# Optimization experiments

Measured on AMD Instinct MI355X. Metric: run time of the kernel, lower is better.

## Reference

```python
import jax, jax.numpy as jnp
from jax import lax
import numpy as np

P_NUM = 63
CHANNEL = 64
KSIZE = 5
PAD = KSIZE // 2
MEAN = jnp.linspace(-310.0, 310.0, P_NUM).reshape(1, 1, P_NUM, 1, 1)
DN = ('NCHW', 'OIHW', 'NCHW')


def rep_pad(x, p=PAD):
    return jnp.pad(x, ((0, 0), (0, 0), (p, p), (p, p)), mode='edge')


def conv(x, w, b):
    out = lax.conv_general_dilated(x, w, (1, 1), 'VALID', dimension_numbers=DN)
    return out + b[None, :, None, None]


def conv_transpose(x, w):
    # torch conv_transpose2d with weight (in, out, k, k), stride 1, no pad ==
    # full correlation with spatially flipped, in/out-transposed kernel
    k = jnp.flip(w, (-2, -1)).transpose(1, 0, 2, 3)  # (out, in, k, k)
    kh = KSIZE - 1
    return lax.conv_general_dilated(x, k, (1, 1), [(kh, kh), (kh, kh)], dimension_numbers=DN)


def crop(x, p=PAD):
    return x[:, :, p:-p, p:-p]


def act(x, w, gradient=False):
    # x: (B,C,H,W); w: (1,C,P,1,1); Gaussian-mixture RBF activation
    d = x[:, :, None, :, :] - MEAN                 # (B,C,P,H,W)
    g = jnp.exp(d * d / -200.0)
    if gradient:
        g = g * (d / -100.0)
    return (g * w).sum(axis=2)                     # (B,C,H,W)


def setup_inputs() -> dict:
    key = jax.random.key(0)
    ks = jax.random.split(key, 8)
    B, H, W = 4, 128, 128
    return {
        'x': jax.random.uniform(ks[0], (B, 1, H, W), jnp.float32),
        'y': jax.random.uniform(ks[1], (B, 1, H, W), jnp.float32),
        'lam': 0,
        'f0': jax.random.normal(ks[2], (CHANNEL, 1, KSIZE, KSIZE), jnp.float32) * 0.1,
        'b0': jax.random.normal(ks[3], (CHANNEL,), jnp.float32) * 0.01,
        'f1': jax.random.normal(ks[4], (1, CHANNEL, KSIZE, KSIZE), jnp.float32) * 0.1,
        'b1': jax.random.normal(ks[5], (1,), jnp.float32) * 0.01,
        'w0': jax.random.normal(ks[6], (1, CHANNEL, P_NUM, 1, 1), jnp.float32) * 0.1,
        'w1': jax.random.normal(ks[7], (1, 1, P_NUM, 1, 1), jnp.float32) * 0.1,
        'lam_param': jnp.float32(np.log(0.1)),
    }


def reference(x, y, lam, f0, b0, f1, b1, w0, w1, lam_param):
    del lam  # third forward arg is ignored by the original module
    x = x * 255.0
    y = y * 255.0
    xx = x
    # encoder
    c0 = conv(rep_pad(x), f0, b0)        # (B,C,H,W)
    a0 = act(c0, w0)
    c1 = conv(rep_pad(a0), f1, b1)       # (B,1,H,W)
    a1 = act(c1, w1)
    # decoder (gradient-like path)
    d = crop(conv_transpose(a1, f1))     # (B,C,H,W)
    d = d * act(c0, w0, gradient=True)
    d = crop(conv_transpose(d, f0))      # (B,1,H,W)
    out = (xx - (d + jnp.exp(lam_param) * (xx - y))) / 255.0
    return out
```

## Files before the change

kernel.cpp:

```cpp
#include <hip/hip_runtime.h>
#include <hip/hip_bf16.h>

#define BSZ 4
#define CH 64
#define IH 128
#define IW 128
#define PN 63
#define PNP 72
#define TLS 32
#define TLH 36
#define XSD 40
#define NT 64
#define CG 2
#define NG 32
#define NPIX (BSZ*IH*IW)

__device__ __forceinline__ void act_vg(float vv, const float* __restrict__ wp,
                                       float& av, float& ag) {
    float pcf = floorf(__fmaf_rn(vv, 0.1f, 31.5f));
    pcf = fminf(fmaxf(pcf, 0.0f), 62.0f);
    const int pc4 = (int)pcf + 4;
    float d0 = vv - __fmaf_rn(pcf, 10.0f, -310.0f);
    d0 = fminf(fmaxf(d0, -150.0f), 150.0f);
    const float G0 = __expf(d0 * d0 * -0.005f);
    const float T  = __expf(d0 * 0.1f);
    const float Ti = __expf(d0 * -0.1f);
    float t0 = wp[pc4] * G0;
    float accv = t0, accg = t0 * d0;
    float Tp = T, Tm = Ti;
    float gc = G0 * 0.60653066f;
    float tp = wp[pc4 + 1] * (gc * Tp), tm = wp[pc4 - 1] * (gc * Tm);
    accv += tp + tm;
    accg = __fmaf_rn(tp, d0 - 10.0f, __fmaf_rn(tm, d0 + 10.0f, accg));
    Tp *= T; Tm *= Ti;
    gc = G0 * 0.13533528f;
    tp = wp[pc4 + 2] * (gc * Tp); tm = wp[pc4 - 2] * (gc * Tm);
    accv += tp + tm;
    accg = __fmaf_rn(tp, d0 - 20.0f, __fmaf_rn(tm, d0 + 20.0f, accg));
    Tp *= T; Tm *= Ti;
    gc = G0 * 0.011108997f;
    tp = wp[pc4 + 3] * (gc * Tp); tm = wp[pc4 - 3] * (gc * Tm);
    accv += tp + tm;
    accg = __fmaf_rn(tp, d0 - 30.0f, __fmaf_rn(tm, d0 + 30.0f, accg));
    av = accv;
    ag = accg * -0.01f;
}

__device__ __forceinline__ float act_v(float vv, const float* __restrict__ wp) {
    float pcf = floorf(__fmaf_rn(vv, 0.1f, 31.5f));
    pcf = fminf(fmaxf(pcf, 0.0f), 62.0f);
    const int pc4 = (int)pcf + 4;
    float d0 = vv - __fmaf_rn(pcf, 10.0f, -310.0f);
    d0 = fminf(fmaxf(d0, -150.0f), 150.0f);
    const float G0 = __expf(d0 * d0 * -0.005f);
    const float T  = __expf(d0 * 0.1f);
    const float Ti = __expf(d0 * -0.1f);
    float accv = wp[pc4] * G0;
    float Tp = T, Tm = Ti;
    accv += G0 * 0.60653066f  * (wp[pc4 + 1] * Tp + wp[pc4 - 1] * Tm);
    Tp *= T; Tm *= Ti;
    accv += G0 * 0.13533528f  * (wp[pc4 + 2] * Tp + wp[pc4 - 2] * Tm);
    Tp *= T; Tm *= Ti;
    accv += G0 * 0.011108997f * (wp[pc4 + 3] * Tp + wp[pc4 - 3] * Tm);
    return accv;
}

__global__ __launch_bounds__(256) void kAB(const float* __restrict__ x,
                                           const float* __restrict__ f0,
                                           const float* __restrict__ b0,
                                           const float* __restrict__ w0,
                                           const float* __restrict__ f1,
                                           float* __restrict__ c1p,
                                           __hip_bfloat16* __restrict__ g0out) {
    __shared__ float xs[XSD * XSD];
    __shared__ float a0s[CG][TLH * TLH];
    __shared__ float w0ps[CG][PNP];

    const int tile = blockIdx.x;
    const int cgi  = blockIdx.y;
    const int cg   = cgi * CG;
    const int b    = tile >> 4;
    const int t    = tile & 15;
    const int h0   = (t >> 2) * TLS;
    const int w0p  = (t & 3) * TLS;
    const int tid  = threadIdx.x;

    for (int i = tid; i < XSD * XSD; i += 256) {
        int iy = i / XSD, ix = i - iy * XSD;
        int gy = min(max(h0 + iy - 4, 0), IH - 1);
        int gx = min(max(w0p + ix - 4, 0), IW - 1);
        xs[i] = x[((size_t)b * IH + gy) * IW + gx] * 255.0f;
    }
    for (int i = tid; i < CG * PNP; i += 256) {
        int cc = i / PNP, k = i - cc * PNP;
        float v = 0.0f;
        if (k >= 4 && k < 4 + PN) v = w0[(size_t)(cg + cc) * PN + (k - 4)];
        w0ps[cc][k] = v;
    }
    __syncthreads();

    for (int p = tid; p < TLH * TLH; p += 256) {
        const int py = p / TLH, px = p - py * TLH;
        const int gy = h0 + py - 2, gx = w0p + px - 2;
        const int gyc = min(max(gy, 0), IH - 1);
        const int gxc = min(max(gx, 0), IW - 1);
        const bool interior = (gy == gyc) && (gx == gxc);
        const int cy = gyc - h0 + 4, cx = gxc - w0p + 4;

        float win[25];
#pragma unroll
        for (int u = 0; u < 5; ++u)
#pragma unroll
            for (int v = 0; v < 5; ++v)
                win[u * 5 + v] = xs[(cy - 2 + u) * XSD + cx - 2 + v];

#pragma unroll
        for (int cc = 0; cc < CG; ++cc) {
            const int c = cg + cc;
            float acc = b0[c];
#pragma unroll
            for (int k = 0; k < 25; ++k)
                acc = __fmaf_rn(win[k], f0[(size_t)c * 25 + k], acc);
            float av, ag;
            act_vg(acc, w0ps[cc], av, ag);
            a0s[cc][p] = av;
            if (interior)
                g0out[(((size_t)b * CH + c) * IH + gy) * IW + gx] = __float2bfloat16(ag);
        }
    }
    __syncthreads();

    const int lx = tid & 15, ly = tid >> 4;
    const int r0 = 2 * ly, c0 = 2 * lx;
    float a00 = 0.f, a01 = 0.f, a10 = 0.f, a11 = 0.f;

#pragma unroll
    for (int cc = 0; cc < CG; ++cc) {
        float win[6][6];
#pragma unroll
        for (int r = 0; r < 6; ++r) {
            const float2* rp = (const float2*)&a0s[cc][(r0 + r) * TLH + c0];
            float2 p0 = rp[0], p1 = rp[1], p2 = rp[2];
            win[r][0] = p0.x; win[r][1] = p0.y; win[r][2] = p1.x;
            win[r][3] = p1.y; win[r][4] = p2.x; win[r][5] = p2.y;
        }
#pragma unroll
        for (int u = 0; u < 5; ++u)
#pragma unroll
            for (int v = 0; v < 5; ++v) {
                const float kv = f1[(size_t)(cg + cc) * 25 + u * 5 + v];
                a00 = __fmaf_rn(win[u][v],         kv, a00);
                a01 = __fmaf_rn(win[u][v + 1],     kv, a01);
                a10 = __fmaf_rn(win[u + 1][v],     kv, a10);
                a11 = __fmaf_rn(win[u + 1][v + 1], kv, a11);
            }
    }

    const int oy = h0 + r0, ox = w0p + c0;
    const size_t base = (size_t)cgi * NPIX + ((size_t)b * IH + oy) * IW + ox;
    *(float2*)&c1p[base]      = make_float2(a00, a01);
    *(float2*)&c1p[base + IW] = make_float2(a10, a11);
}

__global__ __launch_bounds__(256) void kB2(const float* __restrict__ c1p,
                                           const float* __restrict__ b1,
                                           const float* __restrict__ w1,
                                           float* __restrict__ a1) {
    __shared__ float w1p[PNP];
    const int tid = threadIdx.x;
    if (tid < PNP) {
        float v = 0.0f;
        if (tid >= 4 && tid < 4 + PN) v = w1[tid - 4];
        w1p[tid] = v;
    }
    __syncthreads();

    const int pid = blockIdx.x * 256 + tid;
    float vv = b1[0];
#pragma unroll
    for (int g = 0; g < NG; ++g) vv += c1p[(size_t)g * NPIX + pid];
    a1[pid] = act_v(vv, w1p);
}

__global__ __launch_bounds__(256) void kCD(const float* __restrict__ a1,
                                           const float* __restrict__ f1,
                                           const float* __restrict__ f0,
                                           const __hip_bfloat16* __restrict__ g0,
                                           float* __restrict__ d3p) {
    __shared__ float a1s[XSD * XSD];
    __shared__ float dbs[CG][TLH * TLH];

    const int tile = blockIdx.x;
    const int cgi  = blockIdx.y;
    const int cg   = cgi * CG;
    const int b    = tile >> 4;
    const int t    = tile & 15;
    const int h0   = (t >> 2) * TLS;
    const int w0p  = (t & 3) * TLS;
    const int tid  = threadIdx.x;

    for (int p = tid; p < XSD * XSD; p += 256) {
        int iy = p / XSD, ix = p - iy * XSD;
        int gy = h0 + iy - 4, gx = w0p + ix - 4;
        float v = 0.0f;
        if ((unsigned)gy < IH && (unsigned)gx < IW)
            v = a1[((size_t)b * IH + gy) * IW + gx];
        a1s[p] = v;
    }
    __syncthreads();

    for (int p = tid; p < TLH * TLH; p += 256) {
        const int py = p / TLH, px = p - py * TLH;
        const int gy = h0 + py - 2, gx = w0p + px - 2;
        const bool inb = ((unsigned)gy < IH) && ((unsigned)gx < IW);

        float win[25];
#pragma unroll
        for (int u = 0; u < 5; ++u)
#pragma unroll
            for (int v = 0; v < 5; ++v)
                win[u * 5 + v] = a1s[(py + 4 - u) * XSD + (px + 4 - v)];

#pragma unroll
        for (int cc = 0; cc < CG; ++cc) {
            float out = 0.0f;
            if (inb) {
                const int c = cg + cc;
                float d1 = 0.0f;
#pragma unroll
                for (int k = 0; k < 25; ++k)
                    d1 = __fmaf_rn(win[k], f1[(size_t)c * 25 + k], d1);
                out = d1 * __bfloat162float(g0[(((size_t)b * CH + c) * IH + gy) * IW + gx]);
            }
            dbs[cc][p] = out;
        }
    }
    __syncthreads();

    const int lx = tid & 15, ly = tid >> 4;
    const int r0 = 2 * ly, c0 = 2 * lx;
    float a00 = 0.f, a01 = 0.f, a10 = 0.f, a11 = 0.f;

#pragma unroll
    for (int cc = 0; cc < CG; ++cc) {
        float win[6][6];
#pragma unroll
        for (int r = 0; r < 6; ++r) {
            const float2* rp = (const float2*)&dbs[cc][(r0 + r) * TLH + c0];
            float2 p0 = rp[0], p1 = rp[1], p2 = rp[2];
            win[r][0] = p0.x; win[r][1] = p0.y; win[r][2] = p1.x;
            win[r][3] = p1.y; win[r][4] = p2.x; win[r][5] = p2.y;
        }
#pragma unroll
        for (int u = 0; u < 5; ++u)
#pragma unroll
            for (int v = 0; v < 5; ++v) {
                const float kv = f0[(size_t)(cg + cc) * 25 + u * 5 + v];
                a00 = __fmaf_rn(win[4 - u][4 - v], kv, a00);
                a01 = __fmaf_rn(win[4 - u][5 - v], kv, a01);
                a10 = __fmaf_rn(win[5 - u][4 - v], kv, a10);
                a11 = __fmaf_rn(win[5 - u][5 - v], kv, a11);
            }
    }

    const int oy = h0 + r0, ox = w0p + c0;
    const size_t base = (size_t)cgi * NPIX + ((size_t)b * IH + oy) * IW + ox;
    *(float2*)&d3p[base]      = make_float2(a00, a01);
    *(float2*)&d3p[base + IW] = make_float2(a10, a11);
}

__global__ __launch_bounds__(256) void kE(const float* __restrict__ d3p,
                                          const float* __restrict__ x,
                                          const float* __restrict__ y,
                                          const float* __restrict__ lam_param,
                                          float* __restrict__ out) {
    const int pid = blockIdx.x * 256 + threadIdx.x;
    float d3 = 0.0f;
#pragma unroll
    for (int g = 0; g < NG; ++g) d3 += d3p[(size_t)g * NPIX + pid];
    const float elam = __expf(lam_param[0]);
    const float xv = x[pid], yv = y[pid];
    out[pid] = xv - d3 * (1.0f / 255.0f) - elam * (xv - yv);
}

extern "C" void kernel_launch(void* const* d_in, const int* in_sizes, int n_in,
                              void* d_out, int out_size, void* d_ws, size_t ws_size,
                              hipStream_t stream) {
    const float* x   = (const float*)d_in[0];
    const float* y   = (const float*)d_in[1];
    const float* f0  = (const float*)d_in[3];
    const float* b0  = (const float*)d_in[4];
    const float* f1  = (const float*)d_in[5];
    const float* b1  = (const float*)d_in[6];
    const float* w0  = (const float*)d_in[7];
    const float* w1  = (const float*)d_in[8];
    const float* lam = (const float*)d_in[9];
    float* out = (float*)d_out;

    const size_t nch = (size_t)BSZ * CH * IH * IW;
    __hip_bfloat16* g0 = (__hip_bfloat16*)d_ws;
    float* a1  = (float*)(g0 + nch);
    float* c1p = a1 + NPIX;
    float* d3p = c1p + (size_t)NG * NPIX;

    kAB<<<dim3(NT, NG), 256, 0, stream>>>(x, f0, b0, w0, f1, c1p, g0);
    kB2<<<NPIX / 256, 256, 0, stream>>>(c1p, b1, w1, a1);
    kCD<<<dim3(NT, NG), 256, 0, stream>>>(a1, f1, f0, g0, d3p);
    kE <<<NPIX / 256, 256, 0, stream>>>(d3p, x, y, lam, out);
}
```

Baseline: 122.0 us.

## Replace partial-sum buffers with atomics, register-block 2x2 convs, merge final kernel

The per-channel-group partial-sum buffers and their reduction kernels are replaced by float atomicAdd into one accumulator; the encoder accumulator is zeroed with a memset. The epilogue kernel kE is removed: its pointwise term is written by kB2 and the decoder results are atomically added into the output. The first-stage conv and the transpose conv are register-blocked so each thread produces a 2x2 output block from a 6x6 window. The channel group size doubles to 4, halving the grid's y dimension. This cuts global traffic and launches, at the cost of atomic contention and non-deterministic summation order.

```diff
diff --git a/kernel.cpp b/kernel.cpp
--- a/kernel.cpp
+++ b/kernel.cpp
@@ -11,8 +11,9 @@
 #define TLH 36
 #define XSD 40
 #define NT 64
-#define CG 2
-#define NG 32
+#define CG 4
+#define NG 16
+#define NPOS 324
 #define NPIX (BSZ*IH*IW)
 
 __device__ __forceinline__ void act_vg(float vv, const float* __restrict__ wp,
@@ -70,7 +71,7 @@
                                            const float* __restrict__ b0,
                                            const float* __restrict__ w0,
                                            const float* __restrict__ f1,
-                                           float* __restrict__ c1p,
+                                           float* __restrict__ c1acc,
                                            __hip_bfloat16* __restrict__ g0out) {
     __shared__ float xs[XSD * XSD];
     __shared__ float a0s[CG][TLH * TLH];
@@ -99,33 +100,54 @@
     }
     __syncthreads();
 
-    for (int p = tid; p < TLH * TLH; p += 256) {
-        const int py = p / TLH, px = p - py * TLH;
-        const int gy = h0 + py - 2, gx = w0p + px - 2;
-        const int gyc = min(max(gy, 0), IH - 1);
-        const int gxc = min(max(gx, 0), IW - 1);
-        const bool interior = (gy == gyc) && (gx == gxc);
-        const int cy = gyc - h0 + 4, cx = gxc - w0p + 4;
-
-        float win[25];
-#pragma unroll
-        for (int u = 0; u < 5; ++u)
-#pragma unroll
-            for (int v = 0; v < 5; ++v)
-                win[u * 5 + v] = xs[(cy - 2 + u) * XSD + cx - 2 + v];
-
-#pragma unroll
+    for (int p = tid; p < NPOS; p += 256) {
+        const int pyb = p / 18, pxb = p - pyb * 18;
+        const int py = 2 * pyb, px = 2 * pxb;
+        const int gy0 = h0 + py - 2, gx0 = w0p + px - 2;
+        const int gy1 = gy0 + 1,     gx1 = gx0 + 1;
+        const int gyc0 = min(max(gy0, 0), IH - 1), gyc1 = min(max(gy1, 0), IH - 1);
+        const int gxc0 = min(max(gx0, 0), IW - 1), gxc1 = min(max(gx1, 0), IW - 1);
+        const int cy0 = gyc0 - h0 + 4, cx0 = gxc0 - w0p + 4;
+        const int ry1 = (gyc1 - h0 + 4) - cy0;
+        const int rx1 = (gxc1 - w0p + 4) - cx0;
+        const bool iny0 = (gy0 == gyc0), iny1 = (gy1 == gyc1);
+        const bool inx0 = (gx0 == gxc0), inx1 = (gx1 == gxc1);
+
+        float win[6][6];
+#pragma unroll
+        for (int r = 0; r < 6; ++r)
+#pragma unroll
+            for (int c = 0; c < 6; ++c)
+                win[r][c] = xs[(cy0 - 2 + r) * XSD + cx0 - 2 + c];
+
         for (int cc = 0; cc < CG; ++cc) {
             const int c = cg + cc;
-            float acc = b0[c];
-#pragma unroll
-            for (int k = 0; k < 25; ++k)
-                acc = __fmaf_rn(win[k], f0[(size_t)c * 25 + k], acc);
+            const float bias = b0[c];
+            float a00 = bias, a01 = bias, a10 = bias, a11 = bias;
+#pragma unroll
+            for (int u = 0; u < 5; ++u)
+#pragma unroll
+                for (int v = 0; v < 5; ++v) {
+                    const float kv = f0[(size_t)c * 25 + u * 5 + v];
+                    a00 = __fmaf_rn(win[u][v],             kv, a00);
+                    a01 = __fmaf_rn(win[u][rx1 + v],       kv, a01);
+                    a10 = __fmaf_rn(win[ry1 + u][v],       kv, a10);
+                    a11 = __fmaf_rn(win[ry1 + u][rx1 + v], kv, a11);
+                }
             float av, ag;
-            act_vg(acc, w0ps[cc], av, ag);
-            a0s[cc][p] = av;
-            if (interior)
-                g0out[(((size_t)b * CH + c) * IH + gy) * IW + gx] = __float2bfloat16(ag);
+            const size_t gb = ((size_t)b * CH + c) * (IH * IW);
+            act_vg(a00, w0ps[cc], av, ag);
+            a0s[cc][py * TLH + px] = av;
+            if (iny0 && inx0) g0out[gb + gy0 * IW + gx0] = __float2bfloat16(ag);
+            act_vg(a01, w0ps[cc], av, ag);
+            a0s[cc][py * TLH + px + 1] = av;
+            if (iny0 && inx1) g0out[gb + gy0 * IW + gx1] = __float2bfloat16(ag);
+            act_vg(a10, w0ps[cc], av, ag);
+            a0s[cc][(py + 1) * TLH + px] = av;
+            if (iny1 && inx0) g0out[gb + gy1 * IW + gx0] = __float2bfloat16(ag);
+            act_vg(a11, w0ps[cc], av, ag);
+            a0s[cc][(py + 1) * TLH + px + 1] = av;
+            if (iny1 && inx1) g0out[gb + gy1 * IW + gx1] = __float2bfloat16(ag);
         }
     }
     __syncthreads();
@@ -156,16 +178,21 @@
             }
     }
 
-    const int oy = h0 + r0, ox = w0p + c0;
-    const size_t base = (size_t)cgi * NPIX + ((size_t)b * IH + oy) * IW + ox;
-    *(float2*)&c1p[base]      = make_float2(a00, a01);
-    *(float2*)&c1p[base + IW] = make_float2(a10, a11);
-}
-
-__global__ __launch_bounds__(256) void kB2(const float* __restrict__ c1p,
+    const size_t pix = ((size_t)b * IH + h0 + r0) * IW + w0p + c0;
+    atomicAdd(&c1acc[pix],          a00);
+    atomicAdd(&c1acc[pix + 1],      a01);
+    atomicAdd(&c1acc[pix + IW],     a10);
+    atomicAdd(&c1acc[pix + IW + 1], a11);
+}
+
+__global__ __launch_bounds__(256) void kB2(const float* __restrict__ c1acc,
                                            const float* __restrict__ b1,
                                            const float* __restrict__ w1,
-                                           float* __restrict__ a1) {
+                                           const float* __restrict__ x,
+                                           const float* __restrict__ y,
+                                           const float* __restrict__ lam_param,
+                                           float* __restrict__ a1,
+                                           float* __restrict__ out) {
     __shared__ float w1p[PNP];
     const int tid = threadIdx.x;
     if (tid < PNP) {
@@ -176,17 +203,18 @@
     __syncthreads();
 
     const int pid = blockIdx.x * 256 + tid;
-    float vv = b1[0];
-#pragma unroll
-    for (int g = 0; g < NG; ++g) vv += c1p[(size_t)g * NPIX + pid];
-    a1[pid] = act_v(vv, w1p);
+    a1[pid] = act_v(b1[0] + c1acc[pid], w1p);
+
+    const float elam = __expf(lam_param[0]);
+    const float xv = x[pid], yv = y[pid];
+    out[pid] = xv - elam * (xv - yv);
 }
 
 __global__ __launch_bounds__(256) void kCD(const float* __restrict__ a1,
                                            const float* __restrict__ f1,
                                            const float* __restrict__ f0,
                                            const __hip_bfloat16* __restrict__ g0,
-                                           float* __restrict__ d3p) {
+                                           float* __restrict__ out) {
     __shared__ float a1s[XSD * XSD];
     __shared__ float dbs[CG][TLH * TLH];
 
@@ -209,30 +237,45 @@
     }
     __syncthreads();
 
-    for (int p = tid; p < TLH * TLH; p += 256) {
-        const int py = p / TLH, px = p - py * TLH;
-        const int gy = h0 + py - 2, gx = w0p + px - 2;
-        const bool inb = ((unsigned)gy < IH) && ((unsigned)gx < IW);
-
-        float win[25];
-#pragma unroll
-        for (int u = 0; u < 5; ++u)
-#pragma unroll
-            for (int v = 0; v < 5; ++v)
-                win[u * 5 + v] = a1s[(py + 4 - u) * XSD + (px + 4 - v)];
-
-#pragma unroll
+    for (int p = tid; p < NPOS; p += 256) {
+        const int pyb = p / 18, pxb = p - pyb * 18;
+        const int py = 2 * pyb, px = 2 * pxb;
+        const int gy0 = h0 + py - 2, gx0 = w0p + px - 2;
+        const bool iny0 = (unsigned)gy0 < IH, iny1 = (unsigned)(gy0 + 1) < IH;
+        const bool inx0 = (unsigned)gx0 < IW, inx1 = (unsigned)(gx0 + 1) < IW;
+
+        float win[6][6];
+#pragma unroll
+        for (int r = 0; r < 6; ++r) {
+            const float2* rp = (const float2*)&a1s[(py + r) * XSD + px];
+            float2 p0 = rp[0], p1 = rp[1], p2 = rp[2];
+            win[r][0] = p0.x; win[r][1] = p0.y; win[r][2] = p1.x;
+            win[r][3] = p1.y; win[r][4] = p2.x; win[r][5] = p2.y;
+        }
+
         for (int cc = 0; cc < CG; ++cc) {
-            float out = 0.0f;
-            if (inb) {
-                const int c = cg + cc;
-                float d1 = 0.0f;
-#pragma unroll
-                for (int k = 0; k < 25; ++k)
-                    d1 = __fmaf_rn(win[k], f1[(size_t)c * 25 + k], d1);
-                out = d1 * __bfloat162float(g0[(((size_t)b * CH + c) * IH + gy) * IW + gx]);
-            }
-            dbs[cc][p] = out;
+            const int c = cg + cc;
+            float d00 = 0.f, d01 = 0.f, d10 = 0.f, d11 = 0.f;
+#pragma unroll
+            for (int u = 0; u < 5; ++u)
+#pragma unroll
+                for (int v = 0; v < 5; ++v) {
+                    const float kv = f1[(size_t)c * 25 + u * 5 + v];
+                    d00 = __fmaf_rn(win[4 - u][4 - v], kv, d00);
+                    d01 = __fmaf_rn(win[4 - u][5 - v], kv, d01);
+                    d10 = __fmaf_rn(win[5 - u][4 - v], kv, d10);
+                    d11 = __fmaf_rn(win[5 - u][5 - v], kv, d11);
+                }
+            const size_t gb = ((size_t)b * CH + c) * (IH * IW);
+            float o00 = 0.f, o01 = 0.f, o10 = 0.f, o11 = 0.f;
+            if (iny0 && inx0) o00 = d00 * __bfloat162float(g0[gb + gy0 * IW + gx0]);
+            if (iny0 && inx1) o01 = d01 * __bfloat162float(g0[gb + gy0 * IW + gx0 + 1]);
+            if (iny1 && inx0) o10 = d10 * __bfloat162float(g0[gb + (gy0 + 1) * IW + gx0]);
+            if (iny1 && inx1) o11 = d11 * __bfloat162float(g0[gb + (gy0 + 1) * IW + gx0 + 1]);
+            dbs[cc][py * TLH + px]           = o00;
+            dbs[cc][py * TLH + px + 1]       = o01;
+            dbs[cc][(py + 1) * TLH + px]     = o10;
+            dbs[cc][(py + 1) * TLH + px + 1] = o11;
         }
     }
     __syncthreads();
@@ -263,24 +306,12 @@
             }
     }
 
-    const int oy = h0 + r0, ox = w0p + c0;
-    const size_t base = (size_t)cgi * NPIX + ((size_t)b * IH + oy) * IW + ox;
-    *(float2*)&d3p[base]      = make_float2(a00, a01);
-    *(float2*)&d3p[base + IW] = make_float2(a10, a11);
-}
-
-__global__ __launch_bounds__(256) void kE(const float* __restrict__ d3p,
-                                          const float* __restrict__ x,
-                                          const float* __restrict__ y,
-                                          const float* __restrict__ lam_param,
-                                          float* __restrict__ out) {
-    const int pid = blockIdx.x * 256 + threadIdx.x;
-    float d3 = 0.0f;
-#pragma unroll
-    for (int g = 0; g < NG; ++g) d3 += d3p[(size_t)g * NPIX + pid];
-    const float elam = __expf(lam_param[0]);
-    const float xv = x[pid], yv = y[pid];
-    out[pid] = xv - d3 * (1.0f / 255.0f) - elam * (xv - yv);
+    const size_t pix = ((size_t)b * IH + h0 + r0) * IW + w0p + c0;
+    const float s = -1.0f / 255.0f;
+    atomicAdd(&out[pix],          a00 * s);
+    atomicAdd(&out[pix + 1],      a01 * s);
+    atomicAdd(&out[pix + IW],     a10 * s);
+    atomicAdd(&out[pix + IW + 1], a11 * s);
 }
 
 extern "C" void kernel_launch(void* const* d_in, const int* in_sizes, int n_in,
@@ -299,12 +330,11 @@
 
     const size_t nch = (size_t)BSZ * CH * IH * IW;
     __hip_bfloat16* g0 = (__hip_bfloat16*)d_ws;
-    float* a1  = (float*)(g0 + nch);
-    float* c1p = a1 + NPIX;
-    float* d3p = c1p + (size_t)NG * NPIX;
-
-    kAB<<<dim3(NT, NG), 256, 0, stream>>>(x, f0, b0, w0, f1, c1p, g0);
-    kB2<<<NPIX / 256, 256, 0, stream>>>(c1p, b1, w1, a1);
-    kCD<<<dim3(NT, NG), 256, 0, stream>>>(a1, f1, f0, g0, d3p);
-    kE <<<NPIX / 256, 256, 0, stream>>>(d3p, x, y, lam, out);
-}
+    float* c1acc = (float*)(g0 + nch);
+    float* a1    = c1acc + NPIX;
+
+    hipMemsetAsync(c1acc, 0, NPIX * sizeof(float), stream);
+    kAB<<<dim3(NT, NG), 256, 0, stream>>>(x, f0, b0, w0, f1, c1acc, g0);
+    kB2<<<NPIX / 256, 256, 0, stream>>>(c1acc, b1, w1, x, y, lam, a1, out);
+    kCD<<<dim3(NT, NG), 256, 0, stream>>>(a1, f1, f0, g0, out);
+}
```

New measurement: 167.7 us. 1.38x slower.
